# Kernel tuning notes

Measured on AMD Instinct MI355X. Metric: run time of the kernel, lower is better.

## Reference

```python
import jax, jax.numpy as jnp
import numpy as np

N, E, G = 50000, 800000, 128
F_IN, H, NHID, C = 310, 128, 64, 2  # H = 2*nhid
NEG_SLOPE = 0.2


def setup_inputs() -> dict:
    key = jax.random.key(0)
    ks = jax.random.split(key, 16)
    def lin(k, fan_in, shape):
        return (jax.random.normal(k, shape, jnp.float32) / np.sqrt(fan_in)).astype(jnp.float32)
    return {
        "x": jax.random.normal(ks[0], (N, F_IN), jnp.float32),
        "edge_index": jax.random.randint(ks[1], (2, E), 0, N, dtype=jnp.int32),
        "batch": jnp.sort(jax.random.randint(ks[2], (N,), 0, G, dtype=jnp.int32)),
        "W1": lin(ks[3], F_IN, (F_IN, H)),
        "a_src1": lin(ks[4], H, (H,)),
        "a_dst1": lin(ks[5], H, (H,)),
        "b1": jnp.zeros((H,), jnp.float32),
        "W2": lin(ks[6], H, (H, H)),
        "a_src2": lin(ks[7], H, (H,)),
        "a_dst2": lin(ks[8], H, (H,)),
        "b2": jnp.zeros((H,), jnp.float32),
        "fc1_w": lin(ks[9], H, (H, NHID)),
        "fc1_b": jnp.zeros((NHID,), jnp.float32),
        "fc2_w": lin(ks[10], NHID, (NHID, C)),
        "fc2_b": jnp.zeros((C,), jnp.float32),
    }


def _gat(x, src, dst, W, a_src, a_dst, b):
    # PyG GATConv, heads=1: h = xW; e_ij = LeakyReLU(a_src.h_j + a_dst.h_i)
    h = x @ W                               # [N, H]
    asrc = h @ a_src                        # [N]
    adst = h @ a_dst                        # [N]
    e = jax.nn.leaky_relu(asrc[src] + adst[dst], NEG_SLOPE)  # [E']
    # segment softmax over incoming edges of each target node
    m = jax.ops.segment_max(e, dst, num_segments=N)
    ex = jnp.exp(e - m[dst])
    s = jax.ops.segment_sum(ex, dst, num_segments=N)
    w = ex / s[dst]                         # [E']
    out = jax.ops.segment_sum(h[src] * w[:, None], dst, num_segments=N)
    return out + b


def reference(x, edge_index, batch, W1, a_src1, a_dst1, b1,
              W2, a_src2, a_dst2, b2, fc1_w, fc1_b, fc2_w, fc2_b):
    # add self loops (GATConv default add_self_loops=True)
    ar = jnp.arange(N, dtype=edge_index.dtype)
    src = jnp.concatenate([edge_index[0], ar])
    dst = jnp.concatenate([edge_index[1], ar])

    h = jax.nn.selu(_gat(x, src, dst, W1, a_src1, a_dst1, b1))
    h = jax.nn.selu(_gat(h, src, dst, W2, a_src2, a_dst2, b2))

    # global mean pool over graphs
    summed = jax.ops.segment_sum(h, batch, num_segments=G)          # [G, H]
    cnt = jax.ops.segment_sum(jnp.ones((N,), h.dtype), batch, num_segments=G)
    pooled = jax.nn.selu(summed / jnp.maximum(cnt, 1.0)[:, None])

    z = jax.nn.selu(pooled @ fc1_w + fc1_b)  # dropout is identity in eval
    logits = z @ fc2_w + fc2_b
    return jax.nn.log_softmax(logits, axis=-1)
```

## Files before the change

### kernel.cpp

```cpp
#include <hip/hip_runtime.h>
#include <hip/hip_bf16.h>
#include <math.h>

#define NN 50000
#define NE 800000
#define NET (NE + NN)
#define FIN 310
#define HD 128
#define NHID 64
#define NCLS 2
#define NG 128
#define NEG_SLOPE 0.2f
#define KP1 320
#define KP2 128

#define SLOTS 64
#define NPART 8
#define PART_SZ (NN / NPART)
#define EPB 4096
#define NSLICE ((NET + EPB - 1) / EPB)
#define NSC (NSLICE * NPART)
#define GB1 ((NN + 63) / 64)

#define SELU_SCALE 1.0507009873554804934193349852946f
#define SELU_ALPHA 1.6732632423543772848170429916717f

typedef short bf16x8 __attribute__((ext_vector_type(8)));
typedef float f32x4 __attribute__((ext_vector_type(4)));

__device__ __forceinline__ float selu(float x) {
    return SELU_SCALE * (x > 0.f ? x : SELU_ALPHA * (__expf(x) - 1.f));
}
__device__ __forceinline__ float lrelu(float x) {
    return x > 0.f ? x : NEG_SLOPE * x;
}
__device__ __forceinline__ unsigned short f2bf(float f) {
    unsigned int u = __float_as_uint(f);
    u = (u + 0x7fffu + ((u >> 16) & 1u)) >> 16;
    return (unsigned short)u;
}
__device__ __forceinline__ float bf2f(unsigned short b) {
    return __uint_as_float(((unsigned int)b) << 16);
}


__global__ void k_castW(const float* __restrict__ W1, const float* __restrict__ W2,
                        unsigned short* __restrict__ W1p, unsigned short* __restrict__ W2p,
                        int* __restrict__ cursor) {
    int i = blockIdx.x * blockDim.x + threadIdx.x;
    if (i < NN) cursor[i] = 0;
    const int N1 = HD * KP1;
    if (i < N1) {
        int n = i / KP1, k = i % KP1;
        unsigned short v = (k < FIN) ? f2bf(W1[(size_t)k * HD + n]) : (unsigned short)0;
        W1p[((k >> 3) * HD + n) * 8 + (k & 7)] = v;
    } else {
        int j = i - N1;
        if (j < HD * KP2) {
            int n = j / KP2, k = j % KP2;
            W2p[((k >> 3) * HD + n) * 8 + (k & 7)] = f2bf(W2[(size_t)k * HD + n]);
        }
    }
}


#define RGEMM_EPILOGUE                                                         \
    int gr_base = r0 + w * 16 + quad * 4;                                      \
    _Pragma("unroll")                                                          \
    for (int r = 0; r < 4; ++r) {                                              \
        int gr = gr_base + r;                                                  \
        if (gr < M) {                                                          \
            _Pragma("unroll")                                                  \
            for (int nt = 0; nt < 8; ++nt)                                     \
                C[(size_t)gr * HD + nt * 16 + l16] = f2bf(acc[nt][r]);         \
        }                                                                      \
    }                                                                          \
    _Pragma("unroll")                                                          \
    for (int r = 0; r < 4; ++r) {                                              \
        float s1 = 0.f, s2 = 0.f;                                              \
        _Pragma("unroll")                                                      \
        for (int nt = 0; nt < 8; ++nt) {                                       \
            int c = nt * 16 + l16;                                             \
            float v = acc[nt][r];                                              \
            s1 += v * a_src[c];                                                \
            s2 += v * a_dst[c];                                                \
        }                                                                      \
        _Pragma("unroll")                                                      \
        for (int off = 1; off < 16; off <<= 1) {                               \
            s1 += __shfl_xor(s1, off);                                         \
            s2 += __shfl_xor(s2, off);                                         \
        }                                                                      \
        int gr = gr_base + r;                                                  \
        if (l16 == 0 && gr < M) { asrcp[gr] = s1; adstp[gr] = s2; }            \
    }


__global__ __launch_bounds__(256) void k_pre(const float* __restrict__ A,
                                             const unsigned short* __restrict__ Bp,
                                             unsigned short* __restrict__ C,
                                             float* __restrict__ asrcp,
                                             float* __restrict__ adstp,
                                             const float* __restrict__ a_src,
                                             const float* __restrict__ a_dst,
                                             int M,
                                             const int* __restrict__ ei,
                                             int* __restrict__ cursor,
                                             unsigned short* __restrict__ slots) {
    if (blockIdx.x >= GB1) {
        int b = blockIdx.x - GB1;
        int part = b & (NPART - 1);
        int slice = b >> 3;
        int lo = part * PART_SZ;
        int base = slice * EPB + threadIdx.x;
#pragma unroll
        for (int k = 0; k < EPB / 256; ++k) {
            int i = base + k * 256;
            if (i >= NET) break;
            int d = (i < NE) ? ei[NE + i] : (i - NE);
            if ((unsigned)(d - lo) < (unsigned)PART_SZ) {
                int s = (i < NE) ? ei[i] : d;
                int pos = atomicAdd(&cursor[d], 1) & (SLOTS - 1);
                slots[(size_t)d * SLOTS + pos] = (unsigned short)s;
            }
        }
        return;
    }
    int t = threadIdx.x;
    int lane = t & 63, w = t >> 6;
    int quad = lane >> 4, l16 = lane & 15;
    int r0 = blockIdx.x * 64;

    int grow = r0 + w * 16 + l16;
    int arow = min(grow, M - 1);
    const float* aptr = A + (size_t)arow * FIN + quad * 8;

    f32x4 acc[8] = {};
#pragma unroll 2
    for (int k0 = 0; k0 < 288; k0 += 32) {
        const float* ap = aptr + k0;
        float2 f0 = *(const float2*)(ap + 0);
        float2 f1 = *(const float2*)(ap + 2);
        float2 f2 = *(const float2*)(ap + 4);
        float2 f3 = *(const float2*)(ap + 6);
        union { bf16x8 v; unsigned short u[8]; } af;
        af.u[0] = f2bf(f0.x); af.u[1] = f2bf(f0.y);
        af.u[2] = f2bf(f1.x); af.u[3] = f2bf(f1.y);
        af.u[4] = f2bf(f2.x); af.u[5] = f2bf(f2.y);
        af.u[6] = f2bf(f3.x); af.u[7] = f2bf(f3.y);
        const unsigned short* bbase = Bp + ((size_t)(k0 >> 3) + quad) * (HD * 8) + l16 * 8;
#pragma unroll
        for (int nt = 0; nt < 8; ++nt) {
            bf16x8 bfr = *(const bf16x8*)(bbase + nt * 128);
            acc[nt] = __builtin_amdgcn_mfma_f32_16x16x32_bf16(af.v, bfr, acc[nt], 0, 0, 0);
        }
    }
    {
        int kb = 288 + quad * 8;
        union { bf16x8 v; unsigned short u[8]; } af;
#pragma unroll
        for (int j = 0; j < 8; ++j)
            af.u[j] = (kb + j < FIN) ? f2bf(aptr[288 + j]) : (unsigned short)0;
        const unsigned short* bbase = Bp + ((size_t)(288 >> 3) + quad) * (HD * 8) + l16 * 8;
#pragma unroll
        for (int nt = 0; nt < 8; ++nt) {
            bf16x8 bfr = *(const bf16x8*)(bbase + nt * 128);
            acc[nt] = __builtin_amdgcn_mfma_f32_16x16x32_bf16(af.v, bfr, acc[nt], 0, 0, 0);
        }
    }
    RGEMM_EPILOGUE
}


__global__ __launch_bounds__(256) void k_gemm2(const unsigned short* __restrict__ A,
                                               const unsigned short* __restrict__ Bp,
                                               unsigned short* __restrict__ C,
                                               float* __restrict__ asrcp,
                                               float* __restrict__ adstp,
                                               const float* __restrict__ a_src,
                                               const float* __restrict__ a_dst,
                                               int M) {
    int t = threadIdx.x;
    int lane = t & 63, w = t >> 6;
    int quad = lane >> 4, l16 = lane & 15;
    int r0 = blockIdx.x * 64;

    int grow = r0 + w * 16 + l16;
    int arow = min(grow, M - 1);
    const unsigned short* aptr = A + (size_t)arow * KP2 + quad * 8;

    f32x4 acc[8] = {};
#pragma unroll
    for (int k0 = 0; k0 < KP2; k0 += 32) {
        bf16x8 af = *(const bf16x8*)(aptr + k0);
        const unsigned short* bbase = Bp + ((size_t)(k0 >> 3) + quad) * (HD * 8) + l16 * 8;
#pragma unroll
        for (int nt = 0; nt < 8; ++nt) {
            bf16x8 bfr = *(const bf16x8*)(bbase + nt * 128);
            acc[nt] = __builtin_amdgcn_mfma_f32_16x16x32_bf16(af, bfr, acc[nt], 0, 0, 0);
        }
    }
    RGEMM_EPILOGUE
}


__global__ __launch_bounds__(256) void k_gat(const unsigned short* __restrict__ h,
                                             const float* __restrict__ asrc,
                                             const float* __restrict__ adst,
                                             const int* __restrict__ degv,
                                             const unsigned short* __restrict__ slots,
                                             const float* __restrict__ bias,
                                             unsigned short* __restrict__ out) {
    int node = blockIdx.x * 4 + (threadIdx.x >> 6);
    int lane = threadIdx.x & 63;
    if (node >= NN) return;
    int g = lane >> 4, cl = lane & 15;
    int deg = degv[node];
    float adsti = adst[node];

    float2 acc2[4] = {};

    int cnt = min(deg, SLOTS);
    int s_c = 0; float p_c = 0.f;
    if (lane < cnt) {
        s_c = slots[(size_t)node * SLOTS + lane];
        p_c = __expf(lrelu(asrc[s_c] + adsti));
    }
    float den_l = p_c;
    int nt = (cnt + 3) >> 2;
    for (int t = 0; t < nt; t += 2) {
        float pv[2]; uint4 hv[2];
#pragma unroll
        for (int u = 0; u < 2; ++u) {
            int tt = t + u;
            bool valid = tt < nt;
            int e = (4 * tt + g) & 63;
            int s = __shfl(s_c, e);
            float p = __shfl(p_c, e);
            int sa = valid ? s : 0;
            pv[u] = valid ? p : 0.f;
            hv[u] = *(const uint4*)(h + (size_t)sa * HD + cl * 8);
        }
#pragma unroll
        for (int u = 0; u < 2; ++u) {
            float p = pv[u];
            unsigned int w0 = hv[u].x, w1 = hv[u].y, w2 = hv[u].z, w3 = hv[u].w;
            acc2[0].x += p * __uint_as_float(w0 << 16);
            acc2[0].y += p * __uint_as_float(w0 & 0xffff0000u);
            acc2[1].x += p * __uint_as_float(w1 << 16);
            acc2[1].y += p * __uint_as_float(w1 & 0xffff0000u);
            acc2[2].x += p * __uint_as_float(w2 << 16);
            acc2[2].y += p * __uint_as_float(w2 & 0xffff0000u);
            acc2[3].x += p * __uint_as_float(w3 << 16);
            acc2[3].y += p * __uint_as_float(w3 & 0xffff0000u);
        }
    }
#pragma unroll
    for (int k = 0; k < 4; ++k) {
        acc2[k].x += __shfl_xor(acc2[k].x, 16);
        acc2[k].y += __shfl_xor(acc2[k].y, 16);
        acc2[k].x += __shfl_xor(acc2[k].x, 32);
        acc2[k].y += __shfl_xor(acc2[k].y, 32);
    }
#pragma unroll
    for (int off = 32; off; off >>= 1)
        den_l += __shfl_xor(den_l, off);

    if (g == 0) {
        float inv = 1.f / den_l;
        int c0 = cl * 8;
        float4 b0 = *(const float4*)(bias + c0);
        float4 b1 = *(const float4*)(bias + c0 + 4);
        float v0 = selu(acc2[0].x * inv + b0.x);
        float v1 = selu(acc2[0].y * inv + b0.y);
        float v2 = selu(acc2[1].x * inv + b0.z);
        float v3 = selu(acc2[1].y * inv + b0.w);
        float v4 = selu(acc2[2].x * inv + b1.x);
        float v5 = selu(acc2[2].y * inv + b1.y);
        float v6 = selu(acc2[3].x * inv + b1.z);
        float v7 = selu(acc2[3].y * inv + b1.w);
        uint4 pk;
        pk.x = (unsigned int)f2bf(v0) | ((unsigned int)f2bf(v1) << 16);
        pk.y = (unsigned int)f2bf(v2) | ((unsigned int)f2bf(v3) << 16);
        pk.z = (unsigned int)f2bf(v4) | ((unsigned int)f2bf(v5) << 16);
        pk.w = (unsigned int)f2bf(v6) | ((unsigned int)f2bf(v7) << 16);
        *(uint4*)(out + (size_t)node * HD + c0) = pk;
    }
}


__device__ __forceinline__ int lower_bound_i(const int* a, int n, int key) {
    int lo = 0, hi = n;
    while (lo < hi) {
        int mid = (lo + hi) >> 1;
        if (a[mid] < key) lo = mid + 1; else hi = mid;
    }
    return lo;
}

__global__ __launch_bounds__(512) void k_poolfc(const unsigned short* __restrict__ x,
                                                const int* __restrict__ batch,
                                                const float* __restrict__ w1,
                                                const float* __restrict__ b1,
                                                const float* __restrict__ w2,
                                                const float* __restrict__ b2,
                                                float* __restrict__ out) {
    int g = blockIdx.x;
    int t = threadIdx.x;
    __shared__ int lo_s, hi_s;
    __shared__ float red[512];
    __shared__ float pooled_s[128];
    if (t == 0) {
        lo_s = lower_bound_i(batch, NN, g);
        hi_s = lower_bound_i(batch, NN, g + 1);
    }
    __syncthreads();
    int lo = lo_s, hi = hi_s;
    float acc = 0.f;
    for (int n = lo + (t >> 7); n < hi; n += 4)
        acc += bf2f(x[(size_t)n * HD + (t & 127)]);
    red[t] = acc;
    __syncthreads();
    if (t < 128) {
        float v = red[t] + red[t + 128] + red[t + 256] + red[t + 384];
        pooled_s[t] = selu(v / fmaxf((float)(hi - lo), 1.f));
    }
    __syncthreads();
    if (t < 64) {
        float z = 0.f;
#pragma unroll 8
        for (int k = 0; k < HD; ++k) z += pooled_s[k] * w1[k * NHID + t];
        z = selu(z + b1[t]);
        float p0 = z * w2[t * NCLS + 0];
        float p1 = z * w2[t * NCLS + 1];
        for (int off = 32; off; off >>= 1) {
            p0 += __shfl_down(p0, off);
            p1 += __shfl_down(p1, off);
        }
        if (t == 0) {
            float l0 = p0 + b2[0], l1 = p1 + b2[1];
            float m = fmaxf(l0, l1);
            float lse = m + __logf(__expf(l0 - m) + __expf(l1 - m));
            out[g * NCLS + 0] = l0 - lse;
            out[g * NCLS + 1] = l1 - lse;
        }
    }
}


static inline size_t align_up(size_t v, size_t a) { return (v + a - 1) / a * a; }

extern "C" void kernel_launch(void* const* d_in, const int* in_sizes, int n_in,
                              void* d_out, int out_size, void* d_ws, size_t ws_size,
                              hipStream_t stream) {
    const float* x      = (const float*)d_in[0];
    const int*   ei     = (const int*)d_in[1];
    const int*   batch  = (const int*)d_in[2];
    const float* W1     = (const float*)d_in[3];
    const float* a_src1 = (const float*)d_in[4];
    const float* a_dst1 = (const float*)d_in[5];
    const float* b1     = (const float*)d_in[6];
    const float* W2     = (const float*)d_in[7];
    const float* a_src2 = (const float*)d_in[8];
    const float* a_dst2 = (const float*)d_in[9];
    const float* b2     = (const float*)d_in[10];
    const float* fc1_w  = (const float*)d_in[11];
    const float* fc1_b  = (const float*)d_in[12];
    const float* fc2_w  = (const float*)d_in[13];
    const float* fc2_b  = (const float*)d_in[14];
    float* out = (float*)d_out;

    char* ws = (char*)d_ws;
    size_t off = 0;
    unsigned short* h1  = (unsigned short*)(ws + off); off = align_up(off + (size_t)NN * HD * 2, 256);
    unsigned short* o1  = (unsigned short*)(ws + off); off = align_up(off + (size_t)NN * HD * 2, 256);
    float* asrc = (float*)(ws + off); off = align_up(off + (size_t)NN * 4, 256);
    float* adst = (float*)(ws + off); off = align_up(off + (size_t)NN * 4, 256);
    int* cursor = (int*)(ws + off);   off = align_up(off + (size_t)NN * 4, 256);
    unsigned short* slots = (unsigned short*)(ws + off); off = align_up(off + (size_t)NN * SLOTS * 2, 256);
    unsigned short* W1p = (unsigned short*)(ws + off); off = align_up(off + (size_t)HD * KP1 * 2, 256);
    unsigned short* W2p = (unsigned short*)(ws + off); off = align_up(off + (size_t)HD * KP2 * 2, 256);
    (void)ws_size;

    k_castW<<<(HD * (KP1 + KP2) + 255) / 256, 256, 0, stream>>>(W1, W2, W1p, W2p, cursor);

    k_pre<<<GB1 + NSC, 256, 0, stream>>>(x, W1p, h1, asrc, adst, a_src1, a_dst1, NN,
                                         ei, cursor, slots);

    k_gat<<<(NN + 3) / 4, 256, 0, stream>>>(h1, asrc, adst, cursor, slots, b1, o1);

    k_gemm2<<<GB1, 256, 0, stream>>>(o1, W2p, h1, asrc, adst, a_src2, a_dst2, NN);
    k_gat<<<(NN + 3) / 4, 256, 0, stream>>>(h1, asrc, adst, cursor, slots, b2, o1);

    k_poolfc<<<NG, 512, 0, stream>>>(o1, batch, fc1_w, fc1_b, fc2_w, fc2_b, out);
}
```

Baseline: 288.0 us.

## Pack edge indices, prefetch GEMM A-rows, widen GAT gather unroll

k_castW now packs each edge's src/dst pair into one 32-bit word. The 8 partition scatter blocks then read 4 bytes per edge instead of two separate int arrays, and the part index is rotated by block id. The layer-1 GEMM loop is fully unrolled with a one-step register prefetch of the next fp32 A fragment. The GAT aggregation gathers 4 neighbor rows per iteration instead of 2 to raise memory-level parallelism. In exchange, k_castW grows to cover all edges and writes an extra 3.2 MB buffer, and register pressure rises.

```diff
diff --git a/kernel.cpp b/kernel.cpp
--- a/kernel.cpp
+++ b/kernel.cpp
@@ -21,6 +21,7 @@
 #define NSLICE ((NET + EPB - 1) / EPB)
 #define NSC (NSLICE * NPART)
 #define GB1 ((NN + 63) / 64)
+#define CASTW_GRID ((NE + 255) / 256)
 
 #define SELU_SCALE 1.0507009873554804934193349852946f
 #define SELU_ALPHA 1.6732632423543772848170429916717f
@@ -45,8 +46,9 @@
 
 
 __global__ void k_castW(const float* __restrict__ W1, const float* __restrict__ W2,
+                        const int* __restrict__ ei,
                         unsigned short* __restrict__ W1p, unsigned short* __restrict__ W2p,
-                        int* __restrict__ cursor) {
+                        unsigned int* __restrict__ ep, int* __restrict__ cursor) {
     int i = blockIdx.x * blockDim.x + threadIdx.x;
     if (i < NN) cursor[i] = 0;
     const int N1 = HD * KP1;
@@ -54,11 +56,37 @@
         int n = i / KP1, k = i % KP1;
         unsigned short v = (k < FIN) ? f2bf(W1[(size_t)k * HD + n]) : (unsigned short)0;
         W1p[((k >> 3) * HD + n) * 8 + (k & 7)] = v;
-    } else {
+    } else if (i - N1 < HD * KP2) {
         int j = i - N1;
-        if (j < HD * KP2) {
-            int n = j / KP2, k = j % KP2;
-            W2p[((k >> 3) * HD + n) * 8 + (k & 7)] = f2bf(W2[(size_t)k * HD + n]);
+        int n = j / KP2, k = j % KP2;
+        W2p[((k >> 3) * HD + n) * 8 + (k & 7)] = f2bf(W2[(size_t)k * HD + n]);
+    }
+    if (i < NE)
+        ep[i] = ((unsigned int)ei[i] << 16) | (unsigned int)ei[NE + i];
+}
+
+
+__device__ __forceinline__ void scatter_body(int slice, const unsigned int* __restrict__ ep,
+                                             int* __restrict__ cursor,
+                                             unsigned short* __restrict__ slots,
+                                             int part) {
+    int lo = part * PART_SZ;
+    int base = slice * EPB + threadIdx.x;
+#pragma unroll
+    for (int k = 0; k < EPB / 256; ++k) {
+        int i = base + k * 256;
+        if (i >= NET) break;
+        int d, s;
+        if (i < NE) {
+            unsigned int e = ep[i];
+            d = (int)(e & 0xffffu);
+            s = (int)(e >> 16);
+        } else {
+            d = i - NE; s = d;
+        }
+        if ((unsigned)(d - lo) < (unsigned)PART_SZ) {
+            int pos = atomicAdd(&cursor[d], 1) & (SLOTS - 1);
+            slots[(size_t)d * SLOTS + pos] = (unsigned short)s;
         }
     }
 }
@@ -103,26 +131,13 @@
                                              const float* __restrict__ a_src,
                                              const float* __restrict__ a_dst,
                                              int M,
-                                             const int* __restrict__ ei,
+                                             const unsigned int* __restrict__ ep,
                                              int* __restrict__ cursor,
                                              unsigned short* __restrict__ slots) {
     if (blockIdx.x >= GB1) {
         int b = blockIdx.x - GB1;
-        int part = b & (NPART - 1);
-        int slice = b >> 3;
-        int lo = part * PART_SZ;
-        int base = slice * EPB + threadIdx.x;
-#pragma unroll
-        for (int k = 0; k < EPB / 256; ++k) {
-            int i = base + k * 256;
-            if (i >= NET) break;
-            int d = (i < NE) ? ei[NE + i] : (i - NE);
-            if ((unsigned)(d - lo) < (unsigned)PART_SZ) {
-                int s = (i < NE) ? ei[i] : d;
-                int pos = atomicAdd(&cursor[d], 1) & (SLOTS - 1);
-                slots[(size_t)d * SLOTS + pos] = (unsigned short)s;
-            }
-        }
+        int part = (blockIdx.x + 2) & 7;
+        scatter_body(b >> 3, ep, cursor, slots, part);
         return;
     }
     int t = threadIdx.x;
@@ -132,34 +147,41 @@
 
     int grow = r0 + w * 16 + l16;
     int arow = min(grow, M - 1);
-    const float* aptr = A + (size_t)arow * FIN + quad * 8;
+    const float* ap = A + (size_t)arow * FIN + quad * 8;
 
     f32x4 acc[8] = {};
-#pragma unroll 2
+
+    float2 c0 = *(const float2*)(ap + 0);
+    float2 c1 = *(const float2*)(ap + 2);
+    float2 c2 = *(const float2*)(ap + 4);
+    float2 c3 = *(const float2*)(ap + 6);
+#pragma unroll
     for (int k0 = 0; k0 < 288; k0 += 32) {
-        const float* ap = aptr + k0;
-        float2 f0 = *(const float2*)(ap + 0);
-        float2 f1 = *(const float2*)(ap + 2);
-        float2 f2 = *(const float2*)(ap + 4);
-        float2 f3 = *(const float2*)(ap + 6);
+        int kn = (k0 < 256) ? k0 + 32 : 256;
+        float2 n0 = *(const float2*)(ap + kn + 0);
+        float2 n1 = *(const float2*)(ap + kn + 2);
+        float2 n2 = *(const float2*)(ap + kn + 4);
+        float2 n3 = *(const float2*)(ap + kn + 6);
         union { bf16x8 v; unsigned short u[8]; } af;
-        af.u[0] = f2bf(f0.x); af.u[1] = f2bf(f0.y);
-        af.u[2] = f2bf(f1.x); af.u[3] = f2bf(f1.y);
-        af.u[4] = f2bf(f2.x); af.u[5] = f2bf(f2.y);
-        af.u[6] = f2bf(f3.x); af.u[7] = f2bf(f3.y);
+        af.u[0] = f2bf(c0.x); af.u[1] = f2bf(c0.y);
+        af.u[2] = f2bf(c1.x); af.u[3] = f2bf(c1.y);
+        af.u[4] = f2bf(c2.x); af.u[5] = f2bf(c2.y);
+        af.u[6] = f2bf(c3.x); af.u[7] = f2bf(c3.y);
         const unsigned short* bbase = Bp + ((size_t)(k0 >> 3) + quad) * (HD * 8) + l16 * 8;
 #pragma unroll
         for (int nt = 0; nt < 8; ++nt) {
             bf16x8 bfr = *(const bf16x8*)(bbase + nt * 128);
             acc[nt] = __builtin_amdgcn_mfma_f32_16x16x32_bf16(af.v, bfr, acc[nt], 0, 0, 0);
         }
+        c0 = n0; c1 = n1; c2 = n2; c3 = n3;
     }
     {
         int kb = 288 + quad * 8;
+        const float* rp = A + (size_t)arow * FIN;
         union { bf16x8 v; unsigned short u[8]; } af;
 #pragma unroll
         for (int j = 0; j < 8; ++j)
-            af.u[j] = (kb + j < FIN) ? f2bf(aptr[288 + j]) : (unsigned short)0;
+            af.u[j] = (kb + j < FIN) ? f2bf(rp[kb + j]) : (unsigned short)0;
         const unsigned short* bbase = Bp + ((size_t)(288 >> 3) + quad) * (HD * 8) + l16 * 8;
 #pragma unroll
         for (int nt = 0; nt < 8; ++nt) {
@@ -227,10 +249,10 @@
     }
     float den_l = p_c;
     int nt = (cnt + 3) >> 2;
-    for (int t = 0; t < nt; t += 2) {
-        float pv[2]; uint4 hv[2];
-#pragma unroll
-        for (int u = 0; u < 2; ++u) {
+    for (int t = 0; t < nt; t += 4) {
+        float pv[4]; uint4 hv[4];
+#pragma unroll
+        for (int u = 0; u < 4; ++u) {
             int tt = t + u;
             bool valid = tt < nt;
             int e = (4 * tt + g) & 63;
@@ -241,7 +263,7 @@
             hv[u] = *(const uint4*)(h + (size_t)sa * HD + cl * 8);
         }
 #pragma unroll
-        for (int u = 0; u < 2; ++u) {
+        for (int u = 0; u < 4; ++u) {
             float p = pv[u];
             unsigned int w0 = hv[u].x, w1 = hv[u].y, w2 = hv[u].z, w3 = hv[u].w;
             acc2[0].x += p * __uint_as_float(w0 << 16);
@@ -379,12 +401,13 @@
     unsigned short* slots = (unsigned short*)(ws + off); off = align_up(off + (size_t)NN * SLOTS * 2, 256);
     unsigned short* W1p = (unsigned short*)(ws + off); off = align_up(off + (size_t)HD * KP1 * 2, 256);
     unsigned short* W2p = (unsigned short*)(ws + off); off = align_up(off + (size_t)HD * KP2 * 2, 256);
+    unsigned int* epack = (unsigned int*)(ws + off); off = align_up(off + (size_t)NE * 4, 256);
     (void)ws_size;
 
-    k_castW<<<(HD * (KP1 + KP2) + 255) / 256, 256, 0, stream>>>(W1, W2, W1p, W2p, cursor);
+    k_castW<<<CASTW_GRID, 256, 0, stream>>>(W1, W2, ei, W1p, W2p, epack, cursor);
 
     k_pre<<<GB1 + NSC, 256, 0, stream>>>(x, W1p, h1, asrc, adst, a_src1, a_dst1, NN,
-                                         ei, cursor, slots);
+                                         epack, cursor, slots);
 
     k_gat<<<(NN + 3) / 4, 256, 0, stream>>>(h1, asrc, adst, cursor, slots, b1, o1);
 
```

After: 291.1 us, median of 2. About the same (+1.1%).
